# Optimization experiments

Hardware: AMD Instinct MI355X
Metric: run time of the kernel (lower is better)

## Reference

```python
import jax, jax.numpy as jnp
import numpy as np

N_NODES = 100000
N_EDGES = 1600000
D_IN, D_H, D_OUT = 128, 128, 64


def gcn_conv(x, src, dst, W, b, n_nodes):
    """PyG GCNConv (eval): x' = D^{-1/2} (A+I) D^{-1/2} X W + b.
    src/dst already include self-loops."""
    h = x @ W  # [N, d_out] -- transform first (fewer FLOPs when d_out <= d_in)
    deg = jax.ops.segment_sum(jnp.ones_like(dst, dtype=h.dtype), dst, num_segments=n_nodes)
    dinv = jnp.where(deg > 0, jax.lax.rsqrt(deg), 0.0)
    norm = dinv[src] * dinv[dst]  # [E]
    msg = h[src] * norm[:, None]  # gather + scale
    out = jax.ops.segment_sum(msg, dst, num_segments=n_nodes)  # scatter-add
    return out + b


def setup_inputs() -> dict:
    key = jax.random.key(0)
    k = jax.random.split(key, 8)
    x = jax.random.normal(k[0], (N_NODES, D_IN), dtype=jnp.float32)
    edge_index = jax.random.randint(k[1], (2, N_EDGES), 0, N_NODES, dtype=jnp.int32)
    s = 0.1
    W1 = jax.random.normal(k[2], (D_IN, D_H), dtype=jnp.float32) * s
    b1 = jnp.zeros((D_H,), dtype=jnp.float32)
    W2 = jax.random.normal(k[3], (D_H, D_H), dtype=jnp.float32) * s
    b2 = jnp.zeros((D_H,), dtype=jnp.float32)
    W3 = jax.random.normal(k[4], (D_H, D_OUT), dtype=jnp.float32) * s
    b3 = jnp.zeros((D_OUT,), dtype=jnp.float32)
    return {"x": x, "edge_index": edge_index, "W1": W1, "b1": b1,
            "W2": W2, "b2": b2, "W3": W3, "b3": b3}


def reference(x, edge_index, W1, b1, W2, b2, W3, b3):
    n = x.shape[0]
    # add self-loops once (shared by all layers)
    loops = jnp.arange(n, dtype=edge_index.dtype)
    src = jnp.concatenate([edge_index[0], loops])
    dst = jnp.concatenate([edge_index[1], loops])
    h = gcn_conv(x, src, dst, W1, b1, n)
    h = jax.nn.relu(h)  # dropout = identity in eval mode
    h = gcn_conv(h, src, dst, W2, b2, n)
    h = jax.nn.relu(h)
    out = gcn_conv(h, src, dst, W3, b3, n)
    return out
```

## Files before the change

kernel.cpp:

```cpp
#include <hip/hip_runtime.h>
#include <hip/hip_fp16.h>

#define N_NODES 100000
#define N_EDGES 1600000
#define NBUCKET 196
#define CAP     8960
#define EPB     6250

typedef _Float16 half8 __attribute__((ext_vector_type(8)));
typedef float float4v __attribute__((ext_vector_type(4)));

__launch_bounds__(256)
__global__ void k_partition(const int* __restrict__ src, const int* __restrict__ dst,
                            int* __restrict__ bcur, int* __restrict__ ebuf, int E) {
    __shared__ int hist[200];
    __shared__ int basebkt[200];
    const int tid = threadIdx.x;
    if (tid < 200) hist[tid] = 0;
    __syncthreads();
    const int e0 = blockIdx.x * EPB, e1 = min(e0 + EPB, E);
    for (int e = e0 + tid; e < e1; e += 256) atomicAdd(&hist[dst[e] >> 9], 1);
    __syncthreads();
    if (tid < NBUCKET) {
        int h = hist[tid];
        basebkt[tid] = tid * CAP + (h ? atomicAdd(&bcur[tid], h) : 0);
    }
    __syncthreads();
    if (tid < 200) hist[tid] = 0;
    __syncthreads();
    for (int e = e0 + tid; e < e1; e += 256) {
        int d = dst[e];
        int bk = d >> 9;
        int o = atomicAdd(&hist[bk], 1);
        ebuf[basebkt[bk] + o] = (src[e] << 9) | (d & 511);
    }
}

__launch_bounds__(256)
__global__ void k_bsort(const int* __restrict__ ebuf, const int* __restrict__ bcur,
                        int* __restrict__ adj, int* __restrict__ stv,
                        int* __restrict__ deg, float* __restrict__ dinv, int N) {
    __shared__ int cnt[512];
    __shared__ int offs[512];
    const int b = blockIdx.x;
    const int tid = threadIdx.x;
    const int base = b * CAP;
    const int n_b = min(bcur[b], CAP);
    const int node0 = b << 9;
    cnt[tid] = 0; cnt[tid + 256] = 0;
    __syncthreads();
    for (int i = tid; i < n_b; i += 256)
        atomicAdd(&cnt[ebuf[base + i] & 511], 1);
    __syncthreads();
    if (tid < 64) {
        int v[8], tot = 0;
#pragma unroll
        for (int j = 0; j < 8; ++j) { int t = cnt[tid * 8 + j]; v[j] = tot; tot += t; }
        int inc = tot;
#pragma unroll
        for (int d = 1; d < 64; d <<= 1) {
            int u = __shfl_up(inc, d, 64);
            if (tid >= d) inc += u;
        }
        const int excl = inc - tot;
#pragma unroll
        for (int j = 0; j < 8; ++j) offs[tid * 8 + j] = excl + v[j];
    }
    __syncthreads();
#pragma unroll
    for (int h = 0; h < 2; ++h) {
        int local = tid + h * 256;
        int node = node0 + local;
        if (node < N) {
            stv[node] = base + offs[local];
            deg[node] = cnt[local];
            dinv[node] = rsqrtf((float)(cnt[local] + 1));
        }
    }
    __syncthreads();
    for (int i = tid; i < n_b; i += 256) {
        int pk = ebuf[base + i];
        int pos = atomicAdd(&offs[pk & 511], 1);
        adj[base + pos] = pk >> 9;
    }
}

__global__ void k_wswz_all(const float* __restrict__ W1, const float* __restrict__ W2,
                           const float* __restrict__ W3, _Float16* __restrict__ wz1,
                           _Float16* __restrict__ wz2, _Float16* __restrict__ wz3,
                           int* __restrict__ bcur) {
    if (blockIdx.x == 0) bcur[threadIdx.x] = 0;
    int t = blockIdx.x * 256 + threadIdx.x;
    const float* W; _Float16* wsz; int BN;
    if (t < 2048)      { W = W1; wsz = wz1; BN = 128; }
    else if (t < 4096) { W = W2; wsz = wz2; BN = 128; t -= 2048; }
    else if (t < 5120) { W = W3; wsz = wz3; BN = 64;  t -= 4096; }
    else return;
    const int l = t & 63;
    const int kblk = (t >> 6) & 3;
    const int nt = t >> 8;
    const int krow = kblk * 32 + ((l >> 4) << 3);
    const int col = nt * 16 + (l & 15);
    _Float16 v[8];
#pragma unroll
    for (int j = 0; j < 8; ++j) v[j] = (_Float16)W[(krow + j) * BN + col];
    *(uint4*)&wsz[t << 3] = *(uint4*)v;
}

template <int BN, bool AFP16>
__launch_bounds__(256, 4)
__global__ void k_gemm_mfma(const void* __restrict__ Xv, const _Float16* __restrict__ wsz,
                            const float* __restrict__ dinv, __half* __restrict__ out, int N) {
    constexpr int NT = BN / 16;
    constexpr int PAD = 8;
    __shared__ __align__(16) _Float16 smem[BN * 128];

    const int tid = threadIdx.x;
    for (int i = tid; i < BN * 16; i += 256)
        *(uint4*)&smem[i << 3] = *(const uint4*)&wsz[i << 3];

    const int w = tid >> 6;
    const int lane = tid & 63;
    const int q = lane >> 4;
    const int m = lane & 15;
    const int row0 = blockIdx.x * 64;
    const int arow = row0 + w * 16 + m;
    const int arowc = arow < N ? arow : N - 1;

    float4v acc[NT];
#pragma unroll
    for (int nt = 0; nt < NT; ++nt) acc[nt] = (float4v){0.f, 0.f, 0.f, 0.f};

    __syncthreads();

#pragma unroll
    for (int kblk = 0; kblk < 4; ++kblk) {
        half8 af;
        if constexpr (AFP16) {
            const _Float16* A = (const _Float16*)Xv + (size_t)arowc * 128 + (q << 3);
            af = *(const half8*)(A + kblk * 32);
        } else {
            const float* A = (const float*)Xv + (size_t)arowc * 128 + (q << 3);
            float4 a0 = *(const float4*)(A + kblk * 32);
            float4 a1 = *(const float4*)(A + kblk * 32 + 4);
            af[0] = (_Float16)a0.x; af[1] = (_Float16)a0.y;
            af[2] = (_Float16)a0.z; af[3] = (_Float16)a0.w;
            af[4] = (_Float16)a1.x; af[5] = (_Float16)a1.y;
            af[6] = (_Float16)a1.z; af[7] = (_Float16)a1.w;
        }
#pragma unroll
        for (int nt = 0; nt < NT; ++nt) {
            half8 bf = *(const half8*)&smem[(((nt << 2) + kblk) << 9) + (lane << 3)];
            acc[nt] = __builtin_amdgcn_mfma_f32_16x16x32_f16(af, bf, acc[nt], 0, 0, 0);
        }
    }

    float s[4];
#pragma unroll
    for (int r = 0; r < 4; ++r) {
        int rr = row0 + w * 16 + q * 4 + r;
        s[r] = dinv[rr < N ? rr : N - 1];
    }
    __syncthreads();
    _Float16* eb = smem;
#pragma unroll
    for (int nt = 0; nt < NT; ++nt)
#pragma unroll
        for (int r = 0; r < 4; ++r)
            eb[(w * 16 + q * 4 + r) * (BN + PAD) + nt * 16 + m] = (_Float16)(acc[nt][r] * s[r]);
    __syncthreads();
    constexpr int CPR = BN / 8;
    for (int i = tid; i < 64 * CPR; i += 256) {
        int row = i / CPR;
        int cf = (i % CPR) * 8;
        if (row0 + row < N)
            *(uint4*)&out[(size_t)(row0 + row) * BN + cf] = *(uint4*)&eb[row * (BN + PAD) + cf];
    }
}

template <bool RELU>
__launch_bounds__(256)
__global__ void k_agg128(const __half* __restrict__ tp, const int* __restrict__ adj,
                         const int* __restrict__ startv, const int* __restrict__ deg,
                         const float* __restrict__ dinv, const float* __restrict__ bias,
                         _Float16* __restrict__ out, int N) {
    const int node = (blockIdx.x << 2) + (threadIdx.x >> 6);
    const int lane = threadIdx.x & 63;
    if (node >= N) return;
    const int s = startv[node];
    const int cnt = deg[node];
    const float di = dinv[node];
    const int g = lane >> 4;
    const int sl = lane & 15;
    const uint4* rowb = (const uint4*)tp;

    float acc[8] = {0.f, 0.f, 0.f, 0.f, 0.f, 0.f, 0.f, 0.f};
    auto addrow = [&](uint4 v) {
        float2 f0 = __half22float2(*(__half2*)&v.x);
        float2 f1 = __half22float2(*(__half2*)&v.y);
        float2 f2 = __half22float2(*(__half2*)&v.z);
        float2 f3 = __half22float2(*(__half2*)&v.w);
        acc[0] += f0.x; acc[1] += f0.y; acc[2] += f1.x; acc[3] += f1.y;
        acc[4] += f2.x; acc[5] += f2.y; acc[6] += f3.x; acc[7] += f3.y;
    };
    if (g == 0) addrow(rowb[(size_t)node * 16 + sl]);

    int e = 0;
    for (; e + 16 <= cnt; e += 16) {
        int j[4];
#pragma unroll
        for (int u = 0; u < 4; ++u) j[u] = adj[s + e + 4 * u + g];
        uint4 v[4];
#pragma unroll
        for (int u = 0; u < 4; ++u) v[u] = rowb[(size_t)j[u] * 16 + sl];
#pragma unroll
        for (int u = 0; u < 4; ++u) addrow(v[u]);
    }
    for (; e + 4 <= cnt; e += 4)
        addrow(rowb[(size_t)adj[s + e + g] * 16 + sl]);
    if (e + g < cnt)
        addrow(rowb[(size_t)adj[s + e + g] * 16 + sl]);

#pragma unroll
    for (int i = 0; i < 8; ++i) {
        acc[i] += __shfl_xor(acc[i], 32);
        acc[i] += __shfl_xor(acc[i], 16);
    }
    if (g == 0) {
        float4 b0 = *(const float4*)&bias[sl * 8];
        float4 b1 = *(const float4*)&bias[sl * 8 + 4];
        float o[8];
        o[0] = di * acc[0] + b0.x; o[1] = di * acc[1] + b0.y;
        o[2] = di * acc[2] + b0.z; o[3] = di * acc[3] + b0.w;
        o[4] = di * acc[4] + b1.x; o[5] = di * acc[5] + b1.y;
        o[6] = di * acc[6] + b1.z; o[7] = di * acc[7] + b1.w;
        if (RELU)
#pragma unroll
            for (int i = 0; i < 8; ++i) o[i] = fmaxf(o[i], 0.f);
        __half2 ov[4];
#pragma unroll
        for (int i = 0; i < 4; ++i) ov[i] = __floats2half2_rn(o[2 * i], o[2 * i + 1]);
        *(uint4*)&out[(size_t)node * 128 + sl * 8] = *(uint4*)ov;
    }
}

__launch_bounds__(256)
__global__ void k_agg64(const __half* __restrict__ tp, const int* __restrict__ adj,
                        const int* __restrict__ startv, const int* __restrict__ deg,
                        const float* __restrict__ dinv, const float* __restrict__ bias,
                        float* __restrict__ out, int N) {
    const int node = (blockIdx.x << 2) + (threadIdx.x >> 6);
    const int lane = threadIdx.x & 63;
    if (node >= N) return;
    const int s = startv[node];
    const int cnt = deg[node];
    const float di = dinv[node];
    const int g = lane >> 4;
    const int sl = lane & 15;
    const uint2* rowb = (const uint2*)tp;

    float acc[4] = {0.f, 0.f, 0.f, 0.f};
    auto addrow = [&](uint2 v) {
        float2 f0 = __half22float2(*(__half2*)&v.x);
        float2 f1 = __half22float2(*(__half2*)&v.y);
        acc[0] += f0.x; acc[1] += f0.y; acc[2] += f1.x; acc[3] += f1.y;
    };
    if (g == 0) addrow(rowb[(size_t)node * 16 + sl]);

    int e = 0;
    for (; e + 16 <= cnt; e += 16) {
        int j[4];
#pragma unroll
        for (int u = 0; u < 4; ++u) j[u] = adj[s + e + 4 * u + g];
        uint2 v[4];
#pragma unroll
        for (int u = 0; u < 4; ++u) v[u] = rowb[(size_t)j[u] * 16 + sl];
#pragma unroll
        for (int u = 0; u < 4; ++u) addrow(v[u]);
    }
    for (; e + 4 <= cnt; e += 4)
        addrow(rowb[(size_t)adj[s + e + g] * 16 + sl]);
    if (e + g < cnt)
        addrow(rowb[(size_t)adj[s + e + g] * 16 + sl]);

#pragma unroll
    for (int i = 0; i < 4; ++i) {
        acc[i] += __shfl_xor(acc[i], 32);
        acc[i] += __shfl_xor(acc[i], 16);
    }
    if (g == 0) {
        float4 bb = *(const float4*)&bias[sl * 4];
        float4 o;
        o.x = di * acc[0] + bb.x; o.y = di * acc[1] + bb.y;
        o.z = di * acc[2] + bb.z; o.w = di * acc[3] + bb.w;
        *(float4*)&out[(size_t)node * 64 + sl * 4] = o;
    }
}

extern "C" void kernel_launch(void* const* d_in, const int* in_sizes, int n_in,
                              void* d_out, int out_size, void* d_ws, size_t ws_size,
                              hipStream_t stream) {
    const float* x  = (const float*)d_in[0];
    const int*   ei = (const int*)d_in[1];
    const float* W1 = (const float*)d_in[2];
    const float* b1 = (const float*)d_in[3];
    const float* W2 = (const float*)d_in[4];
    const float* b2 = (const float*)d_in[5];
    const float* W3 = (const float*)d_in[6];
    const float* b3 = (const float*)d_in[7];
    float* out = (float*)d_out;
    const int* src = ei;
    const int* dst = ei + N_EDGES;

    char* p = (char*)d_ws;
    __half* tp      = (__half*)p;    p += (size_t)N_NODES * 128 * 2;
    _Float16* hbuf  = (_Float16*)p;  p += (size_t)N_NODES * 128 * 2;
    int*   deg  = (int*)p;    p += (size_t)N_NODES * 4;
    float* dinv = (float*)p;  p += (size_t)N_NODES * 4;
    int*   stv  = (int*)p;    p += (size_t)N_NODES * 4;
    int*   bCur = (int*)p;    p += 1024;
    int*   adj  = (int*)p;    p += (size_t)NBUCKET * CAP * 4 + 16384;
    _Float16* wz1 = (_Float16*)p; p += 16384 * 2;
    _Float16* wz2 = (_Float16*)p; p += 16384 * 2;
    _Float16* wz3 = (_Float16*)p; p += 8192 * 2;
    size_t need = (size_t)(p - (char*)d_ws);
    if (ws_size < need) return;

    int* ebuf = (int*)tp;

    k_wswz_all<<<20, 256, 0, stream>>>(W1, W2, W3, wz1, wz2, wz3, bCur);
    k_partition<<<256, 256, 0, stream>>>(src, dst, bCur, ebuf, N_EDGES);
    k_bsort<<<NBUCKET, 256, 0, stream>>>(ebuf, bCur, adj, stv, deg, dinv, N_NODES);

    const int gb = (N_NODES + 63) / 64;
    const int ab = (N_NODES + 3) / 4;
    k_gemm_mfma<128, false><<<gb, 256, 0, stream>>>(x, wz1, dinv, tp, N_NODES);
    k_agg128<true><<<ab, 256, 0, stream>>>(tp, adj, stv, deg, dinv, b1, hbuf, N_NODES);
    k_gemm_mfma<128, true><<<gb, 256, 0, stream>>>(hbuf, wz2, dinv, tp, N_NODES);
    k_agg128<true><<<ab, 256, 0, stream>>>(tp, adj, stv, deg, dinv, b2, hbuf, N_NODES);
    k_gemm_mfma<64, true><<<gb, 256, 0, stream>>>(hbuf, wz3, dinv, tp, N_NODES);
    k_agg64<<<ab, 256, 0, stream>>>(tp, adj, stv, deg, dinv, b3, out, N_NODES);
}
```

Measured before the change: 360.8 us.

## Transpose MFMA operands to write GEMM output directly, doubling rows per block

The GEMM now swaps the MFMA operands (weights as A, activations as B), so each lane holds four consecutive output columns for one row. That lets the epilogue scale by dinv and store 8-byte chunks straight to global memory, removing the LDS staging buffer and its two barriers. Each wave now processes two 16-row tiles, so a block covers 128 rows and the weight load into LDS is amortized over twice as many rows. The trade-offs are narrower, less coalesced global stores, a dropped occupancy hint in launch_bounds, and half as many blocks.

```diff
diff --git a/kernel.cpp b/kernel.cpp
--- a/kernel.cpp
+++ b/kernel.cpp
@@ -108,11 +108,10 @@
 }
 
 template <int BN, bool AFP16>
-__launch_bounds__(256, 4)
+__launch_bounds__(256)
 __global__ void k_gemm_mfma(const void* __restrict__ Xv, const _Float16* __restrict__ wsz,
                             const float* __restrict__ dinv, __half* __restrict__ out, int N) {
     constexpr int NT = BN / 16;
-    constexpr int PAD = 8;
     __shared__ __align__(16) _Float16 smem[BN * 128];
 
     const int tid = threadIdx.x;
@@ -123,58 +122,50 @@
     const int lane = tid & 63;
     const int q = lane >> 4;
     const int m = lane & 15;
-    const int row0 = blockIdx.x * 64;
-    const int arow = row0 + w * 16 + m;
-    const int arowc = arow < N ? arow : N - 1;
-
-    float4v acc[NT];
-#pragma unroll
-    for (int nt = 0; nt < NT; ++nt) acc[nt] = (float4v){0.f, 0.f, 0.f, 0.f};
-
-    __syncthreads();
-
-#pragma unroll
-    for (int kblk = 0; kblk < 4; ++kblk) {
-        half8 af;
-        if constexpr (AFP16) {
-            const _Float16* A = (const _Float16*)Xv + (size_t)arowc * 128 + (q << 3);
-            af = *(const half8*)(A + kblk * 32);
-        } else {
-            const float* A = (const float*)Xv + (size_t)arowc * 128 + (q << 3);
-            float4 a0 = *(const float4*)(A + kblk * 32);
-            float4 a1 = *(const float4*)(A + kblk * 32 + 4);
-            af[0] = (_Float16)a0.x; af[1] = (_Float16)a0.y;
-            af[2] = (_Float16)a0.z; af[3] = (_Float16)a0.w;
-            af[4] = (_Float16)a1.x; af[5] = (_Float16)a1.y;
-            af[6] = (_Float16)a1.z; af[7] = (_Float16)a1.w;
+    const int row0 = blockIdx.x * 128 + w * 32;
+    __syncthreads();
+
+#pragma unroll
+    for (int t = 0; t < 2; ++t) {
+        const int arow = row0 + t * 16 + m;
+        const int arowc = arow < N ? arow : N - 1;
+
+        float4v acc[NT];
+#pragma unroll
+        for (int nt = 0; nt < NT; ++nt) acc[nt] = (float4v){0.f, 0.f, 0.f, 0.f};
+
+#pragma unroll
+        for (int kblk = 0; kblk < 4; ++kblk) {
+            half8 xf;
+            if constexpr (AFP16) {
+                const _Float16* A = (const _Float16*)Xv + (size_t)arowc * 128 + (q << 3);
+                xf = *(const half8*)(A + kblk * 32);
+            } else {
+                const float* A = (const float*)Xv + (size_t)arowc * 128 + (q << 3);
+                float4 a0 = *(const float4*)(A + kblk * 32);
+                float4 a1 = *(const float4*)(A + kblk * 32 + 4);
+                xf[0] = (_Float16)a0.x; xf[1] = (_Float16)a0.y;
+                xf[2] = (_Float16)a0.z; xf[3] = (_Float16)a0.w;
+                xf[4] = (_Float16)a1.x; xf[5] = (_Float16)a1.y;
+                xf[6] = (_Float16)a1.z; xf[7] = (_Float16)a1.w;
+            }
+#pragma unroll
+            for (int nt = 0; nt < NT; ++nt) {
+                half8 wf = *(const half8*)&smem[(((nt << 2) + kblk) << 9) + (lane << 3)];
+                acc[nt] = __builtin_amdgcn_mfma_f32_16x16x32_f16(wf, xf, acc[nt], 0, 0, 0);
+            }
         }
-#pragma unroll
-        for (int nt = 0; nt < NT; ++nt) {
-            half8 bf = *(const half8*)&smem[(((nt << 2) + kblk) << 9) + (lane << 3)];
-            acc[nt] = __builtin_amdgcn_mfma_f32_16x16x32_f16(af, bf, acc[nt], 0, 0, 0);
+
+        if (arow < N) {
+            const float s = dinv[arow];
+#pragma unroll
+            for (int nt = 0; nt < NT; ++nt) {
+                _Float16 ov[4];
+#pragma unroll
+                for (int r = 0; r < 4; ++r) ov[r] = (_Float16)(acc[nt][r] * s);
+                *(uint2*)&out[(size_t)arow * BN + nt * 16 + q * 4] = *(uint2*)ov;
+            }
         }
-    }
-
-    float s[4];
-#pragma unroll
-    for (int r = 0; r < 4; ++r) {
-        int rr = row0 + w * 16 + q * 4 + r;
-        s[r] = dinv[rr < N ? rr : N - 1];
-    }
-    __syncthreads();
-    _Float16* eb = smem;
-#pragma unroll
-    for (int nt = 0; nt < NT; ++nt)
-#pragma unroll
-        for (int r = 0; r < 4; ++r)
-            eb[(w * 16 + q * 4 + r) * (BN + PAD) + nt * 16 + m] = (_Float16)(acc[nt][r] * s[r]);
-    __syncthreads();
-    constexpr int CPR = BN / 8;
-    for (int i = tid; i < 64 * CPR; i += 256) {
-        int row = i / CPR;
-        int cf = (i % CPR) * 8;
-        if (row0 + row < N)
-            *(uint4*)&out[(size_t)(row0 + row) * BN + cf] = *(uint4*)&eb[row * (BN + PAD) + cf];
     }
 }
 
@@ -332,7 +323,7 @@
     k_partition<<<256, 256, 0, stream>>>(src, dst, bCur, ebuf, N_EDGES);
     k_bsort<<<NBUCKET, 256, 0, stream>>>(ebuf, bCur, adj, stv, deg, dinv, N_NODES);
 
-    const int gb = (N_NODES + 63) / 64;
+    const int gb = (N_NODES + 127) / 128;
     const int ab = (N_NODES + 3) / 4;
     k_gemm_mfma<128, false><<<gb, 256, 0, stream>>>(x, wz1, dinv, tp, N_NODES);
     k_agg128<true><<<ab, 256, 0, stream>>>(tp, adj, stv, deg, dinv, b1, hbuf, N_NODES);
```

New measurement: 371.1 us. 2.8% more time.
